# Kernel optimization log

Measured on AMD Instinct MI355X. Metric: run time of the kernel, lower is better.

The kernel has to match this reference:

```python
import jax, jax.numpy as jnp
import numpy as np

B, S, D = 2, 1024, 2048
H, HKV, HD = 16, 4, 128


def _rotate_half(x):
    x1, x2 = jnp.split(x, 2, axis=-1)
    return jnp.concatenate([-x2, x1], axis=-1)


def setup_inputs() -> dict:
    key = jax.random.key(0)
    ks = jax.random.split(key, 8)
    hidden_states = jax.random.normal(ks[0], (B, S, D), dtype=jnp.float32)
    position_ids = jnp.tile(jnp.arange(S, dtype=jnp.int32)[None, :], (B, 1))
    active_mask = jax.random.bernoulli(ks[1], 0.5, (B, S))
    active_mask = active_mask.at[:, 0].set(True)  # ensure >=1 causal valid key per query
    # standard RoPE tables
    inv_freq = 1.0 / (10000.0 ** (jnp.arange(0, HD, 2, dtype=jnp.float32) / HD))
    freqs = jnp.arange(S, dtype=jnp.float32)[:, None] * inv_freq[None, :]
    emb = jnp.concatenate([freqs, freqs], axis=-1)  # [S, HD]
    cos, sin = jnp.cos(emb), jnp.sin(emb)
    scale = 0.02
    wq = jax.random.normal(ks[2], (D, H * HD), dtype=jnp.float32) * scale
    wk = jax.random.normal(ks[3], (D, HKV * HD), dtype=jnp.float32) * scale
    wv = jax.random.normal(ks[4], (D, HKV * HD), dtype=jnp.float32) * scale
    wo = jax.random.normal(ks[5], (H * HD, D), dtype=jnp.float32) * scale
    return {"hidden_states": hidden_states, "cos": cos, "sin": sin,
            "wq": wq, "wk": wk, "wv": wv, "wo": wo,
            "position_ids": position_ids, "active_mask": active_mask}


def reference(hidden_states, cos, sin, wq, wk, wv, wo, position_ids, active_mask):
    b, s, d = hidden_states.shape
    groups = H // HKV
    scale = HD ** -0.5

    q = (hidden_states @ wq).reshape(b, s, H, HD).transpose(0, 2, 1, 3)    # [b,H,s,hd]
    k = (hidden_states @ wk).reshape(b, s, HKV, HD).transpose(0, 2, 1, 3)  # [b,Hkv,s,hd]
    v = (hidden_states @ wv).reshape(b, s, HKV, HD).transpose(0, 2, 1, 3)

    cs, sn = cos[None, None], sin[None, None]  # [1,1,s,hd]
    q = q * cs + _rotate_half(q) * sn
    k = k * cs + _rotate_half(k) * sn

    # SelectiveKVCache.update_selective (prefill from empty cache):
    # per-batch gather of active tokens, padded (k/v with 0, positions with -1).
    # Padding to full s is math-equivalent to padding to max_active (padded
    # slots are masked with -inf below).
    ar = jnp.arange(s, dtype=jnp.int32)
    order = jnp.argsort(jnp.where(active_mask, ar, ar + s), axis=1)        # actives first, stable order
    sorted_mask = jnp.take_along_axis(active_mask, order, axis=1)          # [b,s]
    gidx = order[:, None, :, None]
    k_sel = jnp.take_along_axis(k, gidx, axis=2) * sorted_mask[:, None, :, None]
    v_sel = jnp.take_along_axis(v, gidx, axis=2) * sorted_mask[:, None, :, None]
    pos_sel = jnp.where(sorted_mask, jnp.take_along_axis(position_ids, order, axis=1), -1)  # [b,s]

    # GQA: repeat kv heads
    k_rep = jnp.repeat(k_sel, groups, axis=1)  # [b,H,skv,hd]
    v_rep = jnp.repeat(v_sel, groups, axis=1)

    scores = jnp.einsum('bhqd,bhkd->bhqk', q, k_rep) * scale
    valid = (pos_sel >= 0)[:, None, None, :]                               # [b,1,1,skv]
    causal = (pos_sel[:, None, :] <= position_ids[:, :, None])[:, None]    # [b,1,q,skv]
    big_neg = jnp.finfo(scores.dtype).min
    scores = jnp.where(valid & causal, scores, big_neg)

    attn = jax.nn.softmax(scores, axis=-1)
    out = jnp.einsum('bhqk,bhkd->bhqd', attn, v_rep)
    out = out.transpose(0, 2, 1, 3).reshape(b, s, H * HD)
    return out @ wo
```

## Files before the change

kernel.cpp:

```cpp
#include <hip/hip_runtime.h>
#include <hip/hip_bf16.h>

#define Bn 2
#define Sn 1024
#define Dn 2048
#define Hn 16
#define HKVn 4
#define HDn 128

typedef __attribute__((ext_vector_type(8))) short s8v;
typedef __attribute__((ext_vector_type(8))) unsigned short u8v;
typedef __attribute__((ext_vector_type(4))) float f4v;
typedef __hip_bfloat16 bf16;

typedef __attribute__((address_space(3))) void lds_void;
typedef __attribute__((address_space(1))) const void gbl_void;
#define ASYNC_LD16(g, l) \
  __builtin_amdgcn_global_load_lds((gbl_void*)(g), (lds_void*)(l), 16, 0, 0)

static __device__ __forceinline__ unsigned short f2b_bits(float f) {
  bf16 h = __float2bfloat16(f);
  return __builtin_bit_cast(unsigned short, h);
}

__global__ void mask_norm(const void* __restrict__ mraw, unsigned char* __restrict__ m8, int n) {
  __shared__ int bytemode;
  if (threadIdx.x == 0) bytemode = 0;
  __syncthreads();
  const unsigned int* mi = (const unsigned int*)mraw;
  int local = 0;
  for (int t = threadIdx.x; t < n / 4; t += blockDim.x)
    if (mi[t] > 1u) local = 1;
  if (local) atomicOr(&bytemode, 1);
  __syncthreads();
  const int bm = bytemode;
  const unsigned char* mb = (const unsigned char*)mraw;
  for (int t = threadIdx.x; t < n; t += blockDim.x)
    m8[t] = bm ? (mb[t] ? 1 : 0) : (mi[t] != 0u ? 1 : 0);
}

__global__ void cvt_bf16(const float* __restrict__ src, bf16* __restrict__ dst, int n8) {
  int stride = gridDim.x * blockDim.x;
  for (int i = blockIdx.x * blockDim.x + threadIdx.x; i < n8; i += stride) {
    float4 a = reinterpret_cast<const float4*>(src)[2 * i];
    float4 b = reinterpret_cast<const float4*>(src)[2 * i + 1];
    u8v o;
    o[0] = f2b_bits(a.x); o[1] = f2b_bits(a.y); o[2] = f2b_bits(a.z); o[3] = f2b_bits(a.w);
    o[4] = f2b_bits(b.x); o[5] = f2b_bits(b.y); o[6] = f2b_bits(b.z); o[7] = f2b_bits(b.w);
    reinterpret_cast<u8v*>(dst)[i] = o;
  }
}

__global__ __launch_bounds__(256) void transpose_w(const float* __restrict__ src,
                                                   bf16* __restrict__ dst, int K, int N) {
  __shared__ float tile[64][65];
  const int bx = blockIdx.x * 64;
  const int by = blockIdx.y * 64;
  const int t = threadIdx.x;
  const int lr = t >> 4, lc4 = (t & 15) * 4;
  #pragma unroll
  for (int it = 0; it < 4; ++it) {
    int k = it * 16 + lr;
    float4 v = *reinterpret_cast<const float4*>(&src[(size_t)(by + k) * N + bx + lc4]);
    tile[k][lc4] = v.x; tile[k][lc4 + 1] = v.y; tile[k][lc4 + 2] = v.z; tile[k][lc4 + 3] = v.w;
  }
  __syncthreads();
  #pragma unroll
  for (int it = 0; it < 4; ++it) {
    int n = it * 16 + lr;
    ushort4 o;
    o.x = f2b_bits(tile[lc4 + 0][n]);
    o.y = f2b_bits(tile[lc4 + 1][n]);
    o.z = f2b_bits(tile[lc4 + 2][n]);
    o.w = f2b_bits(tile[lc4 + 3][n]);
    *reinterpret_cast<ushort4*>(&dst[(size_t)(bx + n) * K + by + lc4]) = o;
  }
}

template <int EPI>
__global__ __launch_bounds__(256) void gemm_nt(
    const bf16* __restrict__ A, const bf16* __restrict__ Bt,
    bf16* __restrict__ Oq, bf16* __restrict__ Ok, bf16* __restrict__ Ov,
    float* __restrict__ Of, int K, int N) {
  __shared__ __align__(16) bf16 Al[128 * 72];
  __shared__ __align__(16) bf16 Bl[128 * 72];
  const int tid = threadIdx.x;
  const int lane = tid & 63, w = tid >> 6;
  const int wm = (w >> 1) * 64, wn = (w & 1) * 64;
  const int m0 = blockIdx.y * 128, n0 = blockIdx.x * 128;
  const int lr = tid >> 3, lc = (tid & 7) * 8;
  const int l16 = lane & 15, lg = lane >> 4;
  f4v acc[4][4] = {};
  for (int k0 = 0; k0 < K; k0 += 64) {
    #pragma unroll
    for (int p = 0; p < 4; ++p) {
      int r = lr + p * 32;
      *reinterpret_cast<float4*>(&Al[r * 72 + lc]) =
          *reinterpret_cast<const float4*>(&A[(size_t)(m0 + r) * K + k0 + lc]);
      *reinterpret_cast<float4*>(&Bl[r * 72 + lc]) =
          *reinterpret_cast<const float4*>(&Bt[(size_t)(n0 + r) * K + k0 + lc]);
    }
    __syncthreads();
    #pragma unroll
    for (int kc = 0; kc < 2; ++kc) {
      s8v af[4], bfr[4];
      #pragma unroll
      for (int mf = 0; mf < 4; ++mf)
        af[mf] = *reinterpret_cast<const s8v*>(&Al[(wm + mf * 16 + l16) * 72 + kc * 32 + lg * 8]);
      #pragma unroll
      for (int nf = 0; nf < 4; ++nf)
        bfr[nf] = *reinterpret_cast<const s8v*>(&Bl[(wn + nf * 16 + l16) * 72 + kc * 32 + lg * 8]);
      #pragma unroll
      for (int mf = 0; mf < 4; ++mf)
        #pragma unroll
        for (int nf = 0; nf < 4; ++nf)
          acc[mf][nf] = __builtin_amdgcn_mfma_f32_16x16x32_bf16(af[mf], bfr[nf], acc[mf][nf], 0, 0, 0);
    }
    __syncthreads();
  }
  #pragma unroll
  for (int mf = 0; mf < 4; ++mf) {
    #pragma unroll
    for (int nf = 0; nf < 4; ++nf) {
      #pragma unroll
      for (int i = 0; i < 4; ++i) {
        int gm = m0 + wm + mf * 16 + lg * 4 + i;
        int gn = n0 + wn + nf * 16 + l16;
        float v = acc[mf][nf][i];
        if (EPI == 0) {
          int b = gm >> 10, s = gm & 1023;
          if (gn < 2048) {
            int h = gn >> 7, hd = gn & 127;
            Oq[(((size_t)(b * Hn + h)) * Sn + s) * HDn + hd] = __float2bfloat16(v);
          } else if (gn < 2560) {
            int t = gn - 2048, kvh = t >> 7, hd = t & 127;
            Ok[(((size_t)(b * HKVn + kvh)) * Sn + s) * HDn + hd] = __float2bfloat16(v);
          } else {
            int t = gn - 2560, kvh = t >> 7, hd = t & 127;
            Ov[(((size_t)(b * HKVn + kvh)) * HDn + hd) * Sn + s] = __float2bfloat16(v);
          }
        } else {
          Of[(size_t)gm * N + gn] = v;
        }
      }
    }
  }
}

__global__ void rope_qk(bf16* __restrict__ qb, bf16* __restrict__ kb,
                        const float* __restrict__ cosp, const float* __restrict__ sinp) {
  const int NQ = Bn * Hn * Sn * 16;
  const int NT = NQ + Bn * HKVn * Sn * 16;
  int stride = gridDim.x * blockDim.x;
  for (int idx = blockIdx.x * blockDim.x + threadIdx.x; idx < NT; idx += stride) {
    bf16* base;
    int rel;
    if (idx < NQ) { base = qb; rel = idx; }
    else          { base = kb; rel = idx - NQ; }
    int d4 = (rel & 15) * 4;
    int s = (rel >> 4) & 1023;
    int head = rel >> 14;
    bf16* p = base + ((size_t)head * Sn + s) * HDn + d4;
    ushort4 a = *reinterpret_cast<ushort4*>(p);
    ushort4 b = *reinterpret_cast<ushort4*>(p + 64);
    float4 c = *reinterpret_cast<const float4*>(&cosp[s * HDn + d4]);
    float4 sv = *reinterpret_cast<const float4*>(&sinp[s * HDn + d4]);
    float x1[4] = {__bfloat162float(__builtin_bit_cast(bf16, a.x)), __bfloat162float(__builtin_bit_cast(bf16, a.y)),
                   __bfloat162float(__builtin_bit_cast(bf16, a.z)), __bfloat162float(__builtin_bit_cast(bf16, a.w))};
    float x2[4] = {__bfloat162float(__builtin_bit_cast(bf16, b.x)), __bfloat162float(__builtin_bit_cast(bf16, b.y)),
                   __bfloat162float(__builtin_bit_cast(bf16, b.z)), __bfloat162float(__builtin_bit_cast(bf16, b.w))};
    float cc[4] = {c.x, c.y, c.z, c.w};
    float ss[4] = {sv.x, sv.y, sv.z, sv.w};
    ushort4 o1, o2;
    unsigned short* o1p = &o1.x; unsigned short* o2p = &o2.x;
    #pragma unroll
    for (int j = 0; j < 4; ++j) {
      o1p[j] = f2b_bits(x1[j] * cc[j] - x2[j] * ss[j]);
      o2p[j] = f2b_bits(x2[j] * cc[j] + x1[j] * ss[j]);
    }
    *reinterpret_cast<ushort4*>(p) = o1;
    *reinterpret_cast<ushort4*>(p + 64) = o2;
  }
}

__global__ __launch_bounds__(256) void attn_fwd(
    const bf16* __restrict__ q, const bf16* __restrict__ k, const bf16* __restrict__ vT,
    const unsigned char* __restrict__ m8, bf16* __restrict__ out) {
  __shared__ __align__(16) bf16 Kl[2][64 * 128];
  __shared__ __align__(16) bf16 Vl[2][128 * 64];
  __shared__ __align__(16) bf16 Pl[4][16 * 72];
  const int tid = threadIdx.x;
  const int lane = tid & 63, w = tid >> 6;
  const int l16 = lane & 15, lg = lane >> 4;
  const int qx = blockIdx.x, h = blockIdx.y, b = blockIdx.z;
  const int NQT = Sn / 64;
  const int qt = (b == 1) ? (NQT - 1 - qx) : qx;
  const int hkv = h >> 2;
  const int q0 = qt * 64 + w * 16;
  const float sl2 = 0.08838834764831845f * 1.44269504088896f;

  const bf16* qp = q + ((size_t)(b * Hn + h) * Sn + q0) * HDn;
  const bf16* kp = k + (size_t)(b * HKVn + hkv) * Sn * HDn;
  const bf16* vp = vT + (size_t)(b * HKVn + hkv) * HDn * Sn;
  const unsigned char* mp = m8 + b * Sn;

  auto stage = [&](int buf, int kbase) {
    #pragma unroll
    for (int i = 0; i < 4; ++i) {
      int ci = i * 256 + w * 64 + lane;
      int kr = ci >> 4, kch = ci & 15;
      ASYNC_LD16(kp + (size_t)(kbase + kr) * HDn + ((kch ^ (kr & 7)) * 8),
                 &Kl[buf][(i * 256 + w * 64) * 8]);
      int vr = ci >> 3, vch = ci & 7;
      ASYNC_LD16(vp + (size_t)vr * Sn + kbase + ((vch ^ (vr & 7)) * 8),
                 &Vl[buf][(i * 256 + w * 64) * 8]);
    }
  };

  s8v qf[4];
  #pragma unroll
  for (int hc = 0; hc < 4; ++hc)
    qf[hc] = *reinterpret_cast<const s8v*>(qp + l16 * HDn + hc * 32 + lg * 8);

  float mrow[4], lrow[4];
  f4v o[8] = {};
  #pragma unroll
  for (int i = 0; i < 4; ++i) { mrow[i] = -1e30f; lrow[i] = 0.f; }

  stage(0, 0);
  __syncthreads();

  for (int kt = 0; kt <= qt; ++kt) {
    const int cur = kt & 1;
    const int kb = kt * 64;
    if (kt < qt) stage(cur ^ 1, kb + 64);

    f4v sc[4] = {};
    #pragma unroll
    for (int ktc = 0; ktc < 4; ++ktc) {
      #pragma unroll
      for (int hc = 0; hc < 4; ++hc) {
        int r = ktc * 16 + l16;
        s8v kf = *reinterpret_cast<const s8v*>(
            &Kl[cur][r * 128 + (((hc * 4 + lg) ^ (r & 7)) * 8)]);
        sc[ktc] = __builtin_amdgcn_mfma_f32_16x16x32_bf16(qf[hc], kf, sc[ktc], 0, 0, 0);
      }
    }
    float pm[4];
    #pragma unroll
    for (int i = 0; i < 4; ++i) pm[i] = -1e30f;
    int act[4];
    #pragma unroll
    for (int ktc = 0; ktc < 4; ++ktc) act[ktc] = mp[kb + ktc * 16 + l16];
    if (kt == qt) {
      #pragma unroll
      for (int ktc = 0; ktc < 4; ++ktc) {
        int j = kb + ktc * 16 + l16;
        #pragma unroll
        for (int i = 0; i < 4; ++i) {
          int qr = q0 + lg * 4 + i;
          float v = sc[ktc][i] * sl2;
          v = (act[ktc] && j <= qr) ? v : -1e30f;
          sc[ktc][i] = v;
          pm[i] = fmaxf(pm[i], v);
        }
      }
    } else {
      #pragma unroll
      for (int ktc = 0; ktc < 4; ++ktc) {
        #pragma unroll
        for (int i = 0; i < 4; ++i) {
          float v = sc[ktc][i] * sl2;
          v = act[ktc] ? v : -1e30f;
          sc[ktc][i] = v;
          pm[i] = fmaxf(pm[i], v);
        }
      }
    }
    #pragma unroll
    for (int off = 1; off < 16; off <<= 1)
      #pragma unroll
      for (int i = 0; i < 4; ++i) pm[i] = fmaxf(pm[i], __shfl_xor(pm[i], off, 64));
    float fac[4];
    #pragma unroll
    for (int i = 0; i < 4; ++i) {
      float mn = fmaxf(mrow[i], pm[i]);
      fac[i] = exp2f(mrow[i] - mn);
      mrow[i] = mn;
    }
    float rs[4] = {0.f, 0.f, 0.f, 0.f};
    #pragma unroll
    for (int ktc = 0; ktc < 4; ++ktc)
      #pragma unroll
      for (int i = 0; i < 4; ++i) {
        float p = exp2f(sc[ktc][i] - mrow[i]);
        rs[i] += p;
        Pl[w][(lg * 4 + i) * 72 + ktc * 16 + l16] = __float2bfloat16(p);
      }
    #pragma unroll
    for (int off = 1; off < 16; off <<= 1)
      #pragma unroll
      for (int i = 0; i < 4; ++i) rs[i] += __shfl_xor(rs[i], off, 64);
    #pragma unroll
    for (int i = 0; i < 4; ++i) lrow[i] = lrow[i] * fac[i] + rs[i];
    #pragma unroll
    for (int fn = 0; fn < 8; ++fn)
      #pragma unroll
      for (int i = 0; i < 4; ++i) o[fn][i] *= fac[i];
    #pragma unroll
    for (int kc = 0; kc < 2; ++kc) {
      s8v pf = *reinterpret_cast<const s8v*>(&Pl[w][l16 * 72 + kc * 32 + lg * 8]);
      #pragma unroll
      for (int fn = 0; fn < 8; ++fn) {
        int d = fn * 16 + l16;
        s8v vf = *reinterpret_cast<const s8v*>(
            &Vl[cur][d * 64 + (((kc * 4 + lg) ^ (d & 7)) * 8)]);
        o[fn] = __builtin_amdgcn_mfma_f32_16x16x32_bf16(pf, vf, o[fn], 0, 0, 0);
      }
    }
    __syncthreads();
  }
  #pragma unroll
  for (int fn = 0; fn < 8; ++fn)
    #pragma unroll
    for (int i = 0; i < 4; ++i) {
      int qr = q0 + lg * 4 + i;
      out[((size_t)b * Sn + qr) * (Hn * HDn) + h * HDn + fn * 16 + l16] =
          __float2bfloat16(o[fn][i] / lrow[i]);
    }
}

extern "C" void kernel_launch(void* const* d_in, const int* in_sizes, int n_in,
                              void* d_out, int out_size, void* d_ws, size_t ws_size,
                              hipStream_t stream) {
  const float* hs   = (const float*)d_in[0];
  const float* cosp = (const float*)d_in[1];
  const float* sinp = (const float*)d_in[2];
  const float* wq   = (const float*)d_in[3];
  const float* wk   = (const float*)d_in[4];
  const float* wv   = (const float*)d_in[5];
  const float* wo   = (const float*)d_in[6];
  const void*  am   = d_in[8];

  char* ws = (char*)d_ws;
  bf16* WT  = (bf16*)(ws);
  bf16* woT = (bf16*)(ws + 12582912);
  bf16* qb  = (bf16*)(ws + 12582912 + 8388608);
  bf16* kb  = (bf16*)(ws + 12582912 + 16777216);
  bf16* vT  = (bf16*)(ws + 12582912 + 18874368);
  bf16* ao  = (bf16*)(ws + 12582912 + 20971520);
  unsigned char* m8 = (unsigned char*)(ws + 12582912 + 29360128);
  bf16* hsb = (bf16*)d_out;
  float* outp = (float*)d_out;

  mask_norm<<<1, 256, 0, stream>>>(am, m8, Bn * Sn);
  cvt_bf16<<<2048, 256, 0, stream>>>(hs, hsb, (Bn * Sn * Dn) / 8);
  transpose_w<<<dim3(32, 32), 256, 0, stream>>>(wq, WT, Dn, 2048);
  transpose_w<<<dim3(8, 32), 256, 0, stream>>>(wk, WT + (size_t)2048 * Dn, Dn, 512);
  transpose_w<<<dim3(8, 32), 256, 0, stream>>>(wv, WT + (size_t)2560 * Dn, Dn, 512);
  transpose_w<<<dim3(32, 32), 256, 0, stream>>>(wo, woT, Dn, 2048);
  gemm_nt<0><<<dim3(24, 16), 256, 0, stream>>>(hsb, WT, qb, kb, vT, nullptr, Dn, 3072);
  rope_qk<<<1024, 256, 0, stream>>>(qb, kb, cosp, sinp);
  attn_fwd<<<dim3(Sn / 64, Hn, Bn), 256, 0, stream>>>(qb, kb, vT, m8, ao);
  gemm_nt<1><<<dim3(16, 16), 256, 0, stream>>>(ao, woT, nullptr, nullptr, nullptr, outp, Hn * HDn, Dn);
}
```

Before: 254.5 us.

## Use async global-to-LDS loads with XOR swizzle in GEMM and merge weight transposes

The GEMM tile loads now use global_load_lds direct-to-LDS 16-byte copies into an unpadded 64-wide tile, with an XOR swizzle on the column chunk to avoid bank conflicts on reads. This removes the register round trip for staging and shrinks LDS usage. The four weight-transpose launches are also merged into one 3D grid launch, with out-of-range blocks exiting early, to cut launch overhead. There is still no double buffering, so the loads are not overlapped with compute.

```diff
diff --git a/kernel.cpp b/kernel.cpp
--- a/kernel.cpp
+++ b/kernel.cpp
@@ -51,10 +51,18 @@
   }
 }
 
-__global__ __launch_bounds__(256) void transpose_w(const float* __restrict__ src,
-                                                   bf16* __restrict__ dst, int K, int N) {
+__global__ __launch_bounds__(256) void transpose_all(
+    const float* __restrict__ s0, const float* __restrict__ s1,
+    const float* __restrict__ s2, const float* __restrict__ s3,
+    bf16* __restrict__ d0, bf16* __restrict__ d1, bf16* __restrict__ d2, bf16* __restrict__ d3) {
   __shared__ float tile[64][65];
+  const int z = blockIdx.z;
+  const float* src = (z == 0) ? s0 : (z == 1) ? s1 : (z == 2) ? s2 : s3;
+  bf16* dst = (z == 0) ? d0 : (z == 1) ? d1 : (z == 2) ? d2 : d3;
+  const int N = (z == 1 || z == 2) ? 512 : 2048;
+  const int K = Dn;
   const int bx = blockIdx.x * 64;
+  if (bx >= N) return;
   const int by = blockIdx.y * 64;
   const int t = threadIdx.x;
   const int lr = t >> 4, lc4 = (t & 15) * 4;
@@ -82,34 +90,39 @@
     const bf16* __restrict__ A, const bf16* __restrict__ Bt,
     bf16* __restrict__ Oq, bf16* __restrict__ Ok, bf16* __restrict__ Ov,
     float* __restrict__ Of, int K, int N) {
-  __shared__ __align__(16) bf16 Al[128 * 72];
-  __shared__ __align__(16) bf16 Bl[128 * 72];
+  __shared__ __align__(16) bf16 Al[128 * 64];
+  __shared__ __align__(16) bf16 Bl[128 * 64];
   const int tid = threadIdx.x;
   const int lane = tid & 63, w = tid >> 6;
   const int wm = (w >> 1) * 64, wn = (w & 1) * 64;
   const int m0 = blockIdx.y * 128, n0 = blockIdx.x * 128;
-  const int lr = tid >> 3, lc = (tid & 7) * 8;
   const int l16 = lane & 15, lg = lane >> 4;
+  const int srow = lane >> 3;
+  const int sch = lane & 7;
   f4v acc[4][4] = {};
   for (int k0 = 0; k0 < K; k0 += 64) {
     #pragma unroll
-    for (int p = 0; p < 4; ++p) {
-      int r = lr + p * 32;
-      *reinterpret_cast<float4*>(&Al[r * 72 + lc]) =
-          *reinterpret_cast<const float4*>(&A[(size_t)(m0 + r) * K + k0 + lc]);
-      *reinterpret_cast<float4*>(&Bl[r * 72 + lc]) =
-          *reinterpret_cast<const float4*>(&Bt[(size_t)(n0 + r) * K + k0 + lc]);
+    for (int i = 0; i < 4; ++i) {
+      const int rb = w * 32 + i * 8;
+      const int r = rb + srow;
+      const int cs = (sch ^ (r & 7)) * 8;
+      ASYNC_LD16(&A[(size_t)(m0 + r) * K + k0 + cs], &Al[rb * 64]);
+      ASYNC_LD16(&Bt[(size_t)(n0 + r) * K + k0 + cs], &Bl[rb * 64]);
     }
     __syncthreads();
     #pragma unroll
     for (int kc = 0; kc < 2; ++kc) {
       s8v af[4], bfr[4];
       #pragma unroll
-      for (int mf = 0; mf < 4; ++mf)
-        af[mf] = *reinterpret_cast<const s8v*>(&Al[(wm + mf * 16 + l16) * 72 + kc * 32 + lg * 8]);
-      #pragma unroll
-      for (int nf = 0; nf < 4; ++nf)
-        bfr[nf] = *reinterpret_cast<const s8v*>(&Bl[(wn + nf * 16 + l16) * 72 + kc * 32 + lg * 8]);
+      for (int mf = 0; mf < 4; ++mf) {
+        int r = wm + mf * 16 + l16;
+        af[mf] = *reinterpret_cast<const s8v*>(&Al[r * 64 + (((kc * 4 + lg) ^ (r & 7)) * 8)]);
+      }
+      #pragma unroll
+      for (int nf = 0; nf < 4; ++nf) {
+        int r = wn + nf * 16 + l16;
+        bfr[nf] = *reinterpret_cast<const s8v*>(&Bl[r * 64 + (((kc * 4 + lg) ^ (r & 7)) * 8)]);
+      }
       #pragma unroll
       for (int mf = 0; mf < 4; ++mf)
         #pragma unroll
@@ -355,10 +368,8 @@
 
   mask_norm<<<1, 256, 0, stream>>>(am, m8, Bn * Sn);
   cvt_bf16<<<2048, 256, 0, stream>>>(hs, hsb, (Bn * Sn * Dn) / 8);
-  transpose_w<<<dim3(32, 32), 256, 0, stream>>>(wq, WT, Dn, 2048);
-  transpose_w<<<dim3(8, 32), 256, 0, stream>>>(wk, WT + (size_t)2048 * Dn, Dn, 512);
-  transpose_w<<<dim3(8, 32), 256, 0, stream>>>(wv, WT + (size_t)2560 * Dn, Dn, 512);
-  transpose_w<<<dim3(32, 32), 256, 0, stream>>>(wo, woT, Dn, 2048);
+  transpose_all<<<dim3(32, 32, 4), 256, 0, stream>>>(
+      wq, wk, wv, wo, WT, WT + (size_t)2048 * Dn, WT + (size_t)2560 * Dn, woT);
   gemm_nt<0><<<dim3(24, 16), 256, 0, stream>>>(hsb, WT, qb, kb, vT, nullptr, Dn, 3072);
   rope_qk<<<1024, 256, 0, stream>>>(qb, kb, cosp, sinp);
   attn_fwd<<<dim3(Sn / 64, Hn, Bn), 256, 0, stream>>>(qb, kb, vT, m8, ao);
```

New measurement: 246.8 us. -3.0%, faster.
